# Optimization experiments

Measured on AMD Instinct MI355X. Metric: run time of the kernel, lower is better.

Reference implementation:

```python
import jax, jax.numpy as jnp
import numpy as np

TEMPERATURE = 0.1
EPS = 1e-8

# MatchingRuleAllViews defaults:
#   intra_view_same_class=1, intra_view_different_class=0,
#   inter_view_same_class=1, inter_view_different_class=0,
#   inter_image_same_class=-1, inter_image_different_class=-1,
#   self_similarity=-1

def setup_inputs() -> dict:
    key = jax.random.key(0)
    k1, k2, k3 = jax.random.split(key, 3)
    B, V, C, HW = 2, 2, 64, 1024
    student = jax.random.normal(k1, (B, V, C, HW), dtype=jnp.float32)
    teacher = jax.random.normal(k2, (B, V, C, HW), dtype=jnp.float32)
    labels = jax.random.randint(k3, (B, V, HW), 0, 5, dtype=jnp.int32)
    return {"student_embeddings": student, "teacher_embeddings": teacher, "labels": labels}


def _masks(B, V, HW, labels_flat):
    # image / view / pixel ids for each of the N = B*V*HW flattened positions
    image_ids = jnp.repeat(jnp.arange(B), V * HW)          # [N]
    view_ids = jnp.tile(jnp.repeat(jnp.arange(V), HW), B)  # [N]
    pixel_ids = jnp.tile(jnp.arange(HW), B * V)            # [N]
    si = image_ids[:, None] == image_ids[None, :]
    sv = view_ids[:, None] == view_ids[None, :]
    sp = pixel_ids[:, None] == pixel_ids[None, :]
    sc = labels_flat[:, None] == labels_flat[None, :]
    # default rule: same image -> (same class ? 1 : 0); different image -> -1;
    # self-similarity (same image, view, pixel) -> -1
    mask = jnp.where(si, jnp.where(sc, 1, 0), -1)
    mask = jnp.where(si & sv & sp, -1, mask)
    numerator_mask = (mask == 1).astype(jnp.float32)
    denom_mask = (mask >= 0).astype(jnp.float32)
    return numerator_mask, denom_mask


def reference(student_embeddings, teacher_embeddings, labels):
    B, V, C, HW = student_embeddings.shape
    N = B * V * HW
    # [B,V,C,HW] -> [N,C], L2-normalized
    sf = student_embeddings.transpose(0, 1, 3, 2).reshape(N, C)
    tf = teacher_embeddings.transpose(0, 1, 3, 2).reshape(N, C)
    sf = sf / jnp.linalg.norm(sf, axis=1, keepdims=True).clip(1e-12)
    tf = tf / jnp.linalg.norm(tf, axis=1, keepdims=True).clip(1e-12)
    logits = (sf @ tf.T) / TEMPERATURE  # [N,N]

    labels_flat = labels.reshape(-1)
    numerator_mask, denom_mask = _masks(B, V, HW, labels_flat)

    # masked log-softmax over dim 1 (denominator restricted to denom_mask)
    masked_logits = jnp.where(denom_mask > 0, logits, -jnp.inf)
    log_prob = jax.nn.log_softmax(masked_logits, axis=1)
    log_prob = jnp.where(jnp.isneginf(log_prob), 0.0, log_prob)

    numerator_sums = numerator_mask.sum(1)
    mean_log_prob_pos = (numerator_mask * log_prob).sum(1) / (numerator_sums + EPS)
    valid = numerator_sums > EPS  # [N] bool
    n_valid = valid.sum().astype(jnp.float32)
    loss = -jnp.sum(jnp.where(valid, mean_log_prob_pos, 0.0)) / n_valid

    # bg_anchors=False branch: (loss * non_bg[valid]).sum() / (non_bg[valid].sum() + eps)
    non_bg = (labels_flat != 0).astype(jnp.float32)
    non_bg_valid_sum = jnp.sum(non_bg * valid.astype(jnp.float32))
    loss = (loss * non_bg_valid_sum) / (non_bg_valid_sum + EPS)
    return loss
```

## Files before the change

kernel.cpp:

```cpp
#include <hip/hip_runtime.h>
#include <math.h>

#define NEG_INF (-1e30f)

typedef __attribute__((ext_vector_type(8))) short s16x8;
typedef __attribute__((ext_vector_type(4))) float f32x4;

__device__ __forceinline__ unsigned int pack_bf16(float lo, float hi) {
    unsigned int ul = __float_as_uint(lo);
    ul += 0x7FFFu + ((ul >> 16) & 1u);
    unsigned int uh = __float_as_uint(hi);
    uh += 0x7FFFu + ((uh >> 16) & 1u);
    return (ul >> 16) | (uh & 0xFFFF0000u);
}

__global__ __launch_bounds__(256) void prep_kernel(
    const float* __restrict__ s, const float* __restrict__ t,
    unsigned int* __restrict__ sbf, unsigned int* __restrict__ tbf,
    float* __restrict__ accums) {
    const int b = blockIdx.x;
    const int tid = threadIdx.x;
    const int n0 = (b & 63) << 6;
    const float* __restrict__ src = (b >= 64) ? t : s;
    unsigned int* __restrict__ dst = (b >= 64) ? tbf : sbf;

    if (b == 0 && tid < 8) accums[tid] = 0.f;

    __shared__ __align__(16) float lds[64][68];
    __shared__ float red[4][64];
    __shared__ float rinv[64];

    {
        const int cg = tid & 15;
        const int pos4 = (tid >> 4) << 2;
        const int base = ((n0 >> 10) << 16) + (n0 & 1023) + pos4;
#pragma unroll
        for (int cc = 0; cc < 4; ++cc) {
            const int c = (cg << 2) + cc;
            float4 v = *(const float4*)(src + base + (c << 10));
            lds[pos4 + 0][c] = v.x;
            lds[pos4 + 1][c] = v.y;
            lds[pos4 + 2][c] = v.z;
            lds[pos4 + 3][c] = v.w;
        }
    }
    __syncthreads();

    {
        const int pos = tid & 63;
        const int q = tid >> 6;
        float ssq = 0.f;
#pragma unroll
        for (int j = 0; j < 4; ++j) {
            float4 v = *(const float4*)&lds[pos][(q << 4) + (j << 2)];
            ssq = fmaf(v.x, v.x, ssq);
            ssq = fmaf(v.y, v.y, ssq);
            ssq = fmaf(v.z, v.z, ssq);
            ssq = fmaf(v.w, v.w, ssq);
        }
        red[q][pos] = ssq;
    }
    __syncthreads();
    if (tid < 64) {
        float v = red[0][tid] + red[1][tid] + red[2][tid] + red[3][tid];
        rinv[tid] = 1.f / fmaxf(sqrtf(v), 1e-12f);
    }
    __syncthreads();

    {
        const int pos = tid >> 2;
        const int o0 = (tid & 3) << 1;
        const float r = rinv[pos];
        unsigned int* drow = dst + ((n0 + pos) << 5);
#pragma unroll
        for (int oo = 0; oo < 2; ++oo) {
            const int o = o0 + oo;
            const float* lp = &lds[pos][o << 3];
            uint4 u;
            u.x = pack_bf16(lp[0] * r, lp[1] * r);
            u.y = pack_bf16(lp[2] * r, lp[3] * r);
            u.z = pack_bf16(lp[4] * r, lp[5] * r);
            u.w = pack_bf16(lp[6] * r, lp[7] * r);
            *(uint4*)(drow + (o << 2)) = u;
        }
    }
}

__global__ __launch_bounds__(256, 2) void main_kernel(
    const s16x8* __restrict__ sbf, const s16x8* __restrict__ tbf,
    const int* __restrict__ labels, float4* __restrict__ stats) {

    const int rb = blockIdx.x >> 4;
    const int jc = blockIdx.x & 15;
    const int img = rb >> 4;
    const int i0 = rb * 128;
    const int jb = img * 2048 + jc * 128;

    const int tid = threadIdx.x;
    const int lane = tid & 63;
    const int wv = tid >> 6;
    const int warow = wv << 5;
    const int quad = lane >> 4;
    const int col16 = lane & 15;

    s16x8 afr[2][2];
#pragma unroll
    for (int rt = 0; rt < 2; ++rt) {
        const int row = i0 + warow + 16 * rt + col16;
#pragma unroll
        for (int kh = 0; kh < 2; ++kh)
            afr[rt][kh] = sbf[row * 8 + quad + 4 * kh];
    }
    s16x8 bfr[8][2];
#pragma unroll
    for (int ct = 0; ct < 8; ++ct) {
        const int col = jb + 16 * ct + col16;
#pragma unroll
        for (int kh = 0; kh < 2; ++kh)
            bfr[ct][kh] = tbf[col * 8 + quad + 4 * kh];
    }

    int labi[8], ig[8];
#pragma unroll
    for (int rt = 0; rt < 2; ++rt)
#pragma unroll
        for (int reg = 0; reg < 4; ++reg) {
            const int rr = rt * 4 + reg;
            ig[rr] = i0 + warow + 16 * rt + 4 * quad + reg;
            labi[rr] = labels[ig[rr]];
        }
    int lj[8];
#pragma unroll
    for (int ct = 0; ct < 8; ++ct) lj[ct] = labels[jb + 16 * ct + col16];

    float s_sum[8], A_sum[8], c_sum[8];
#pragma unroll
    for (int rr = 0; rr < 8; ++rr) { s_sum[rr] = 0.f; A_sum[rr] = 0.f; c_sum[rr] = 0.f; }

#pragma unroll
    for (int ct = 0; ct < 8; ++ct) {
        const int jg = jb + 16 * ct + col16;
#pragma unroll
        for (int rt = 0; rt < 2; ++rt) {
            f32x4 z = {0.f, 0.f, 0.f, 0.f};
            z = __builtin_amdgcn_mfma_f32_16x16x32_bf16(afr[rt][0], bfr[ct][0], z, 0, 0, 0);
            z = __builtin_amdgcn_mfma_f32_16x16x32_bf16(afr[rt][1], bfr[ct][1], z, 0, 0, 0);
#pragma unroll
            for (int reg = 0; reg < 4; ++reg) {
                const int rr = rt * 4 + reg;
                float logit = z[reg] * 10.f;
                bool self = (jg == ig[rr]);
                float e = __expf((self ? NEG_INF : logit) - 10.f);
                s_sum[rr] += e;
                if (!self && lj[ct] == labi[rr]) { A_sum[rr] += logit; c_sum[rr] += 1.f; }
            }
        }
    }

#pragma unroll
    for (int off = 1; off < 16; off <<= 1)
#pragma unroll
        for (int rr = 0; rr < 8; ++rr) {
            s_sum[rr] += __shfl_xor(s_sum[rr], off, 64);
            A_sum[rr] += __shfl_xor(A_sum[rr], off, 64);
            c_sum[rr] += __shfl_xor(c_sum[rr], off, 64);
        }

    if (col16 == 0) {
#pragma unroll
        for (int rr = 0; rr < 8; ++rr)
            stats[ig[rr] * 16 + jc] = make_float4(s_sum[rr], A_sum[rr], c_sum[rr], 0.f);
    }
}

__global__ __launch_bounds__(256) void finalize_kernel(
    const float4* __restrict__ stats, const int* __restrict__ labels,
    float* __restrict__ accums, float* __restrict__ out) {
    const int tid = threadIdx.x;
    const int r = blockIdx.x * 256 + tid;

    float ssum = 0.f, A = 0.f, cnt = 0.f;
#pragma unroll
    for (int c = 0; c < 16; ++c) {
        float4 v = stats[r * 16 + c];
        ssum += v.x; A += v.y; cnt += v.z;
    }
    float mlpp = 0.f, val = 0.f, nbv = 0.f;
    if (cnt > 0.5f) {
        float lse = 10.f + __logf(ssum);
        mlpp = (A - cnt * lse) / (cnt + 1e-8f);
        val = 1.f;
        nbv = (labels[r] != 0) ? 1.f : 0.f;
    }

    __shared__ float red0[256], red1[256], red2[256];
    red0[tid] = mlpp; red1[tid] = val; red2[tid] = nbv;
    __syncthreads();
    for (int off = 128; off > 0; off >>= 1) {
        if (tid < off) {
            red0[tid] += red0[tid + off];
            red1[tid] += red1[tid + off];
            red2[tid] += red2[tid + off];
        }
        __syncthreads();
    }

    if (tid == 0) {
        atomicAdd(&accums[0], red0[0]);
        atomicAdd(&accums[1], red1[0]);
        atomicAdd(&accums[2], red2[0]);
        __threadfence();
        unsigned int old = atomicAdd((unsigned int*)&accums[3], 1u);
        if (old == 15u) {
            float S = atomicAdd(&accums[0], 0.f);
            float V = atomicAdd(&accums[1], 0.f);
            float NB = atomicAdd(&accums[2], 0.f);
            float loss = -S / V;
            out[0] = loss * NB / (NB + 1e-8f);
        }
    }
}

extern "C" void kernel_launch(void* const* d_in, const int* in_sizes, int n_in,
                              void* d_out, int out_size, void* d_ws, size_t ws_size,
                              hipStream_t stream) {
    const float* s = (const float*)d_in[0];
    const float* t = (const float*)d_in[1];
    const int* labels = (const int*)d_in[2];
    float* out = (float*)d_out;

    char* ws = (char*)d_ws;
    float* accums = (float*)ws;
    unsigned int* sbf = (unsigned int*)(ws + 1024);
    unsigned int* tbf = (unsigned int*)(ws + 1024 + 524288);
    float4* stats = (float4*)(ws + 1024 + 2 * 524288);

    hipLaunchKernelGGL(prep_kernel, dim3(128), dim3(256), 0, stream,
                       s, t, sbf, tbf, accums);
    hipLaunchKernelGGL(main_kernel, dim3(512), dim3(256), 0, stream,
                       (const s16x8*)sbf, (const s16x8*)tbf, labels, stats);
    hipLaunchKernelGGL(finalize_kernel, dim3(16), dim3(256), 0, stream,
                       stats, labels, accums, out);
}
```

Baseline: 76.59 us.

## Fuse finalize into main kernel with per-row-block full-row reduction

The main kernel is restructured so each 512-thread block owns 16 anchor rows and sweeps the full 2048-column same-image range, reducing row statistics in LDS instead of writing partial stats to global memory. The finalize kernel is removed, and the per-row loss terms are accumulated with atomics plus a last-block counter in the main kernel. This removes one kernel launch and the stats round-trip, but cuts the grid to 256 blocks with less A-fragment reuse per wave and serialises more work per wave.

New measurement: 83.47 us. +9.0%, slower.

```diff
diff --git a/kernel.cpp b/kernel.cpp
--- a/kernel.cpp
+++ b/kernel.cpp
@@ -86,137 +86,108 @@
     }
 }
 
-__global__ __launch_bounds__(256, 2) void main_kernel(
+__global__ __launch_bounds__(512) void mainrow_kernel(
     const s16x8* __restrict__ sbf, const s16x8* __restrict__ tbf,
-    const int* __restrict__ labels, float4* __restrict__ stats) {
-
-    const int rb = blockIdx.x >> 4;
-    const int jc = blockIdx.x & 15;
-    const int img = rb >> 4;
-    const int i0 = rb * 128;
-    const int jb = img * 2048 + jc * 128;
-
+    const int* __restrict__ labels, float* __restrict__ accums,
+    float* __restrict__ out) {
+
+    const int b = blockIdx.x;
+    const int i0 = b << 4;
+    const int img = b >> 7;
     const int tid = threadIdx.x;
     const int lane = tid & 63;
     const int wv = tid >> 6;
-    const int warow = wv << 5;
     const int quad = lane >> 4;
     const int col16 = lane & 15;
 
-    s16x8 afr[2][2];
-#pragma unroll
-    for (int rt = 0; rt < 2; ++rt) {
-        const int row = i0 + warow + 16 * rt + col16;
-#pragma unroll
-        for (int kh = 0; kh < 2; ++kh)
-            afr[rt][kh] = sbf[row * 8 + quad + 4 * kh];
-    }
-    s16x8 bfr[8][2];
-#pragma unroll
-    for (int ct = 0; ct < 8; ++ct) {
-        const int col = jb + 16 * ct + col16;
-#pragma unroll
-        for (int kh = 0; kh < 2; ++kh)
-            bfr[ct][kh] = tbf[col * 8 + quad + 4 * kh];
-    }
-
-    int labi[8], ig[8];
-#pragma unroll
-    for (int rt = 0; rt < 2; ++rt)
+    s16x8 a0 = sbf[(i0 + col16) * 8 + quad];
+    s16x8 a1 = sbf[(i0 + col16) * 8 + quad + 4];
+
+    int ig[4], labi[4];
+#pragma unroll
+    for (int reg = 0; reg < 4; ++reg) {
+        ig[reg] = i0 + 4 * quad + reg;
+        labi[reg] = labels[ig[reg]];
+    }
+
+    float ssum[4] = {0.f, 0.f, 0.f, 0.f};
+    float Asum[4] = {0.f, 0.f, 0.f, 0.f};
+    float csum[4] = {0.f, 0.f, 0.f, 0.f};
+
+    const int colbase = img * 2048 + (wv << 8) + col16;
+#pragma unroll 4
+    for (int ct = 0; ct < 16; ++ct) {
+        const int col = colbase + (ct << 4);
+        s16x8 b0 = tbf[col * 8 + quad];
+        s16x8 b1 = tbf[col * 8 + quad + 4];
+        const int lj = labels[col];
+        f32x4 z = {0.f, 0.f, 0.f, 0.f};
+        z = __builtin_amdgcn_mfma_f32_16x16x32_bf16(a0, b0, z, 0, 0, 0);
+        z = __builtin_amdgcn_mfma_f32_16x16x32_bf16(a1, b1, z, 0, 0, 0);
 #pragma unroll
         for (int reg = 0; reg < 4; ++reg) {
-            const int rr = rt * 4 + reg;
-            ig[rr] = i0 + warow + 16 * rt + 4 * quad + reg;
-            labi[rr] = labels[ig[rr]];
-        }
-    int lj[8];
-#pragma unroll
-    for (int ct = 0; ct < 8; ++ct) lj[ct] = labels[jb + 16 * ct + col16];
-
-    float s_sum[8], A_sum[8], c_sum[8];
-#pragma unroll
-    for (int rr = 0; rr < 8; ++rr) { s_sum[rr] = 0.f; A_sum[rr] = 0.f; c_sum[rr] = 0.f; }
-
-#pragma unroll
-    for (int ct = 0; ct < 8; ++ct) {
-        const int jg = jb + 16 * ct + col16;
-#pragma unroll
-        for (int rt = 0; rt < 2; ++rt) {
-            f32x4 z = {0.f, 0.f, 0.f, 0.f};
-            z = __builtin_amdgcn_mfma_f32_16x16x32_bf16(afr[rt][0], bfr[ct][0], z, 0, 0, 0);
-            z = __builtin_amdgcn_mfma_f32_16x16x32_bf16(afr[rt][1], bfr[ct][1], z, 0, 0, 0);
-#pragma unroll
-            for (int reg = 0; reg < 4; ++reg) {
-                const int rr = rt * 4 + reg;
-                float logit = z[reg] * 10.f;
-                bool self = (jg == ig[rr]);
-                float e = __expf((self ? NEG_INF : logit) - 10.f);
-                s_sum[rr] += e;
-                if (!self && lj[ct] == labi[rr]) { A_sum[rr] += logit; c_sum[rr] += 1.f; }
+            float logit = z[reg] * 10.f;
+            bool self = (col == ig[reg]);
+            float e = __expf((self ? NEG_INF : logit) - 10.f);
+            ssum[reg] += e;
+            if (!self && lj == labi[reg]) { Asum[reg] += logit; csum[reg] += 1.f; }
+        }
+    }
+
+#pragma unroll
+    for (int off = 1; off < 16; off <<= 1)
+#pragma unroll
+        for (int reg = 0; reg < 4; ++reg) {
+            ssum[reg] += __shfl_xor(ssum[reg], off, 64);
+            Asum[reg] += __shfl_xor(Asum[reg], off, 64);
+            csum[reg] += __shfl_xor(csum[reg], off, 64);
+        }
+
+    __shared__ float part[3][8][16];
+    if (col16 == 0) {
+#pragma unroll
+        for (int reg = 0; reg < 4; ++reg) {
+            part[0][wv][4 * quad + reg] = ssum[reg];
+            part[1][wv][4 * quad + reg] = Asum[reg];
+            part[2][wv][4 * quad + reg] = csum[reg];
+        }
+    }
+    __syncthreads();
+
+    if (tid < 16) {
+        float S = 0.f, A = 0.f, C = 0.f;
+#pragma unroll
+        for (int w = 0; w < 8; ++w) {
+            S += part[0][w][tid];
+            A += part[1][w][tid];
+            C += part[2][w][tid];
+        }
+        float bm = 0.f, bv = 0.f, bn = 0.f;
+        if (C > 0.5f) {
+            float lse = 10.f + __logf(S);
+            bm = (A - C * lse) / (C + 1e-8f);
+            bv = 1.f;
+            bn = (labels[i0 + tid] != 0) ? 1.f : 0.f;
+        }
+#pragma unroll
+        for (int off = 1; off < 16; off <<= 1) {
+            bm += __shfl_xor(bm, off, 64);
+            bv += __shfl_xor(bv, off, 64);
+            bn += __shfl_xor(bn, off, 64);
+        }
+        if (tid == 0) {
+            atomicAdd(&accums[0], bm);
+            atomicAdd(&accums[1], bv);
+            atomicAdd(&accums[2], bn);
+            __threadfence();
+            unsigned int old = atomicAdd((unsigned int*)&accums[3], 1u);
+            if (old == 255u) {
+                float Sm = atomicAdd(&accums[0], 0.f);
+                float V  = atomicAdd(&accums[1], 0.f);
+                float NB = atomicAdd(&accums[2], 0.f);
+                float loss = -Sm / V;
+                out[0] = loss * NB / (NB + 1e-8f);
             }
-        }
-    }
-
-#pragma unroll
-    for (int off = 1; off < 16; off <<= 1)
-#pragma unroll
-        for (int rr = 0; rr < 8; ++rr) {
-            s_sum[rr] += __shfl_xor(s_sum[rr], off, 64);
-            A_sum[rr] += __shfl_xor(A_sum[rr], off, 64);
-            c_sum[rr] += __shfl_xor(c_sum[rr], off, 64);
-        }
-
-    if (col16 == 0) {
-#pragma unroll
-        for (int rr = 0; rr < 8; ++rr)
-            stats[ig[rr] * 16 + jc] = make_float4(s_sum[rr], A_sum[rr], c_sum[rr], 0.f);
-    }
-}
-
-__global__ __launch_bounds__(256) void finalize_kernel(
-    const float4* __restrict__ stats, const int* __restrict__ labels,
-    float* __restrict__ accums, float* __restrict__ out) {
-    const int tid = threadIdx.x;
-    const int r = blockIdx.x * 256 + tid;
-
-    float ssum = 0.f, A = 0.f, cnt = 0.f;
-#pragma unroll
-    for (int c = 0; c < 16; ++c) {
-        float4 v = stats[r * 16 + c];
-        ssum += v.x; A += v.y; cnt += v.z;
-    }
-    float mlpp = 0.f, val = 0.f, nbv = 0.f;
-    if (cnt > 0.5f) {
-        float lse = 10.f + __logf(ssum);
-        mlpp = (A - cnt * lse) / (cnt + 1e-8f);
-        val = 1.f;
-        nbv = (labels[r] != 0) ? 1.f : 0.f;
-    }
-
-    __shared__ float red0[256], red1[256], red2[256];
-    red0[tid] = mlpp; red1[tid] = val; red2[tid] = nbv;
-    __syncthreads();
-    for (int off = 128; off > 0; off >>= 1) {
-        if (tid < off) {
-            red0[tid] += red0[tid + off];
-            red1[tid] += red1[tid + off];
-            red2[tid] += red2[tid + off];
-        }
-        __syncthreads();
-    }
-
-    if (tid == 0) {
-        atomicAdd(&accums[0], red0[0]);
-        atomicAdd(&accums[1], red1[0]);
-        atomicAdd(&accums[2], red2[0]);
-        __threadfence();
-        unsigned int old = atomicAdd((unsigned int*)&accums[3], 1u);
-        if (old == 15u) {
-            float S = atomicAdd(&accums[0], 0.f);
-            float V = atomicAdd(&accums[1], 0.f);
-            float NB = atomicAdd(&accums[2], 0.f);
-            float loss = -S / V;
-            out[0] = loss * NB / (NB + 1e-8f);
         }
     }
 }
@@ -233,12 +204,9 @@
     float* accums = (float*)ws;
     unsigned int* sbf = (unsigned int*)(ws + 1024);
     unsigned int* tbf = (unsigned int*)(ws + 1024 + 524288);
-    float4* stats = (float4*)(ws + 1024 + 2 * 524288);
 
     hipLaunchKernelGGL(prep_kernel, dim3(128), dim3(256), 0, stream,
                        s, t, sbf, tbf, accums);
-    hipLaunchKernelGGL(main_kernel, dim3(512), dim3(256), 0, stream,
-                       (const s16x8*)sbf, (const s16x8*)tbf, labels, stats);
-    hipLaunchKernelGGL(finalize_kernel, dim3(16), dim3(256), 0, stream,
-                       stats, labels, accums, out);
-}
+    hipLaunchKernelGGL(mainrow_kernel, dim3(256), dim3(512), 0, stream,
+                       (const s16x8*)sbf, (const s16x8*)tbf, labels, accums, out);
+}
```
